# Kernel tuning notes

Measured on AMD Instinct MI355X. Metric: run time of the kernel, lower is better.

## Reference

```python
import jax, jax.numpy as jnp
import numpy as np

DIM = 1024
NUM_HEADS = 16
HEAD_DIM = DIM // NUM_HEADS
SCALE = HEAD_DIM ** -0.5


def setup_inputs() -> dict:
    key = jax.random.key(0)
    ks = jax.random.split(key, 6)
    B, N, C = 2, 2048, DIM
    std = 1.0 / np.sqrt(C)
    x = jax.random.normal(ks[0], (B, N, C), dtype=jnp.float32)
    wq = jax.random.normal(ks[1], (C, C), dtype=jnp.float32) * std
    wk = jax.random.normal(ks[2], (C, C), dtype=jnp.float32) * std
    wv = jax.random.normal(ks[3], (C, C), dtype=jnp.float32) * std
    w_proj = jax.random.normal(ks[4], (C, C), dtype=jnp.float32) * std
    b_proj = jax.random.normal(ks[5], (C,), dtype=jnp.float32) * 0.01
    return {"x": x, "wq": wq, "wk": wk, "wv": wv, "w_proj": w_proj, "b_proj": b_proj}


def reference(x, wq, wk, wv, w_proj, b_proj):
    B, N, C = x.shape
    H, D = NUM_HEADS, HEAD_DIM
    Nq = N // 2
    # q from first half of tokens; k, v from all tokens
    q = (x[:, :Nq] @ wq.T).reshape(B, Nq, H, D).transpose(0, 2, 1, 3)  # [B,H,Nq,D]
    k = (x @ wk.T).reshape(B, N, H, D).transpose(0, 2, 1, 3)           # [B,H,N,D]
    v = (x @ wv.T).reshape(B, N, H, D).transpose(0, 2, 1, 3)           # [B,H,N,D]
    attn = jnp.einsum('bhqd,bhkd->bhqk', q, k) * SCALE
    attn = jax.nn.softmax(attn, axis=-1)
    out = jnp.einsum('bhqk,bhkd->bhqd', attn, v)                       # [B,H,Nq,D]
    out = out.transpose(0, 2, 1, 3).reshape(B, Nq, C)
    return out @ w_proj.T + b_proj
```

## Files before the change

### kernel.cpp

```cpp
#include <hip/hip_runtime.h>

typedef _Float16 f16;
typedef _Float16 f16x8 __attribute__((ext_vector_type(8)));
typedef _Float16 f16x4 __attribute__((ext_vector_type(4)));
typedef float f32x4 __attribute__((ext_vector_type(4)));

#define MFMA_F16(a, b, c) __builtin_amdgcn_mfma_f32_16x16x32_f16(a, b, c, 0, 0, 0)

__device__ __forceinline__ void gld16(const void* g, void* l) {
  __builtin_amdgcn_global_load_lds(
      (const __attribute__((address_space(1))) unsigned int*)(unsigned long long)g,
      (__attribute__((address_space(3))) unsigned int*)(unsigned long long)l, 16, 0, 0);
}

__global__ __launch_bounds__(256) void cvt_x_kernel(const float* __restrict__ in,
                                                    f16* __restrict__ out, int n8) {
  int i = blockIdx.x * 256 + threadIdx.x;
  if (i >= n8) return;
  const float4* p = (const float4*)(in + (size_t)i * 8);
  float4 a = p[0], b = p[1];
  f16x8 o = {(f16)a.x, (f16)a.y, (f16)a.z, (f16)a.w,
             (f16)b.x, (f16)b.y, (f16)b.z, (f16)b.w};
  *(f16x8*)(out + (size_t)i * 8) = o;
}

__global__ __launch_bounds__(256) void cvt_w4_kernel(const float* __restrict__ w0,
                                                     const float* __restrict__ w1,
                                                     const float* __restrict__ w2,
                                                     const float* __restrict__ w3,
                                                     f16* __restrict__ out) {
  int i = blockIdx.x * 256 + threadIdx.x;
  int t = i >> 17, r = i & 131071;
  const float* w = (t == 0) ? w0 : (t == 1) ? w1 : (t == 2) ? w2 : w3;
  const float4* p = (const float4*)(w + (size_t)r * 8);
  float4 a = p[0], b = p[1];
  f16x8 o = {(f16)a.x, (f16)a.y, (f16)a.z, (f16)a.w,
             (f16)b.x, (f16)b.y, (f16)b.z, (f16)b.w};
  *(f16x8*)(out + (size_t)t * 1048576 + (size_t)r * 8) = o;
}

__global__ __launch_bounds__(256) void qkv_gemm_kernel(
    const f16* __restrict__ A, const f16* __restrict__ Wq,
    const f16* __restrict__ Wk, const f16* __restrict__ Wv,
    f16* __restrict__ Qo, f16* __restrict__ Ko, f16* __restrict__ VT) {
  __shared__ __align__(16) f16 As[2][64 * 64];
  __shared__ __align__(16) f16 Bs[2][128 * 64];
  const int bid = blockIdx.x + blockIdx.y * 8;
  const int swz = (bid & 7) * 160 + (bid >> 3);
  const int bx = swz & 7, y = swz >> 3;
  const f16* Bw;
  f16* Co = nullptr;
  int mt, isv = 0;
  if (y < 32) { Bw = Wq; Co = Qo; mt = (y & 15) | ((y >> 4) << 5); }
  else if (y < 96) { Bw = Wk; Co = Ko; mt = y - 32; }
  else { Bw = Wv; isv = 1; mt = y - 96; }
  const int m0 = mt * 64, n0 = bx * 128;
  const int tid = threadIdx.x, lane = tid & 63, w = tid >> 6;
  const int wr = w >> 1, wc = w & 1, g = lane >> 4, c = lane & 15;
  const int r_st = tid >> 3, t_st = tid & 7;

  auto stage = [&](int k0, int buf) {
#pragma unroll
    for (int i = 0; i < 2; ++i) {
      int row = r_st + i * 32;
      int sl = (t_st ^ (row & 7)) * 8;
      gld16(&A[(size_t)(m0 + row) * 1024 + k0 + sl], &As[buf][(row * 8 + t_st) * 8]);
    }
#pragma unroll
    for (int i = 0; i < 4; ++i) {
      int row = r_st + i * 32;
      int sl = (t_st ^ (row & 7)) * 8;
      gld16(&Bw[(size_t)(n0 + row) * 1024 + k0 + sl], &Bs[buf][(row * 8 + t_st) * 8]);
    }
  };

  f32x4 acc[2][4] = {};

  stage(0, 0);
  __syncthreads();

  for (int t = 0; t < 16; ++t) {
    const int cur = t & 1;
    if (t < 15) stage((t + 1) * 64, cur ^ 1);
#pragma unroll
    for (int kb = 0; kb < 2; ++kb) {
      f16x8 af[2], bf[4];
      const int sw = ((kb * 4 + g) ^ (c & 7)) * 8;
#pragma unroll
      for (int m2 = 0; m2 < 2; ++m2)
        af[m2] = *(const f16x8*)&As[cur][(wr * 32 + m2 * 16 + c) * 64 + sw];
#pragma unroll
      for (int nt = 0; nt < 4; ++nt)
        bf[nt] = *(const f16x8*)&Bs[cur][(wc * 64 + nt * 16 + c) * 64 + sw];
#pragma unroll
      for (int m2 = 0; m2 < 2; ++m2)
#pragma unroll
        for (int nt = 0; nt < 4; ++nt)
          acc[m2][nt] = MFMA_F16(af[m2], bf[nt], acc[m2][nt]);
    }
    __syncthreads();
  }

  if (isv) {
    const int b = m0 >> 11;
    const int n_base = (m0 & 2047) + wr * 32 + g * 4;
#pragma unroll
    for (int m2 = 0; m2 < 2; ++m2)
#pragma unroll
      for (int nt = 0; nt < 4; ++nt) {
        int col = n0 + wc * 64 + nt * 16 + c;
        int h = col >> 6, d = col & 63;
        f16x4 pv = {(f16)acc[m2][nt][0], (f16)acc[m2][nt][1],
                    (f16)acc[m2][nt][2], (f16)acc[m2][nt][3]};
        *(f16x4*)&VT[((size_t)((b * 16 + h) * 64 + d)) * 2048 + n_base + m2 * 16] = pv;
      }
  } else {
#pragma unroll
    for (int m2 = 0; m2 < 2; ++m2)
#pragma unroll
      for (int nt = 0; nt < 4; ++nt) {
        int col = n0 + wc * 64 + nt * 16 + c;
#pragma unroll
        for (int r = 0; r < 4; ++r)
          Co[(size_t)(m0 + wr * 32 + m2 * 16 + g * 4 + r) * 1024 + col] =
              (f16)acc[m2][nt][r];
      }
  }
}

__global__ __launch_bounds__(256) void proj_gemm_kernel(
    const f16* __restrict__ A, const f16* __restrict__ Bw,
    float* __restrict__ C) {
  __shared__ __align__(16) f16 As[2][64 * 64];
  __shared__ __align__(16) f16 Bs[2][64 * 64];
  const int bid = blockIdx.x;
  const int swz = (bid & 7) * 128 + (bid >> 3);
  const int n0 = (swz & 15) * 64, m0 = ((swz >> 4) & 31) * 64;
  const int kbase = (swz >> 9) * 512;
  const int tid = threadIdx.x, lane = tid & 63, w = tid >> 6;
  const int wr = w >> 1, wc = w & 1, g = lane >> 4, c = lane & 15;
  const int r_st = tid >> 3, t_st = tid & 7;

  auto stage = [&](int k0, int buf) {
#pragma unroll
    for (int i = 0; i < 2; ++i) {
      int row = r_st + i * 32;
      int sl = (t_st ^ (row & 7)) * 8;
      gld16(&A[(size_t)(m0 + row) * 1024 + k0 + sl], &As[buf][(row * 8 + t_st) * 8]);
      gld16(&Bw[(size_t)(n0 + row) * 1024 + k0 + sl], &Bs[buf][(row * 8 + t_st) * 8]);
    }
  };

  f32x4 acc[2][2] = {};

  stage(kbase, 0);
  __syncthreads();

  for (int t = 0; t < 8; ++t) {
    const int cur = t & 1;
    if (t < 7) stage(kbase + (t + 1) * 64, cur ^ 1);
#pragma unroll
    for (int kb = 0; kb < 2; ++kb) {
      f16x8 af[2], bf[2];
      const int sw = ((kb * 4 + g) ^ (c & 7)) * 8;
#pragma unroll
      for (int m2 = 0; m2 < 2; ++m2)
        af[m2] = *(const f16x8*)&As[cur][(wr * 32 + m2 * 16 + c) * 64 + sw];
#pragma unroll
      for (int nt = 0; nt < 2; ++nt)
        bf[nt] = *(const f16x8*)&Bs[cur][(wc * 32 + nt * 16 + c) * 64 + sw];
#pragma unroll
      for (int m2 = 0; m2 < 2; ++m2)
#pragma unroll
        for (int nt = 0; nt < 2; ++nt)
          acc[m2][nt] = MFMA_F16(af[m2], bf[nt], acc[m2][nt]);
    }
    __syncthreads();
  }

#pragma unroll
  for (int m2 = 0; m2 < 2; ++m2)
#pragma unroll
    for (int nt = 0; nt < 2; ++nt) {
      int col = n0 + wc * 32 + nt * 16 + c;
#pragma unroll
      for (int r = 0; r < 4; ++r)
        unsafeAtomicAdd(&C[(size_t)(m0 + wr * 32 + m2 * 16 + g * 4 + r) * 1024 + col],
                        acc[m2][nt][r]);
    }
}

__global__ __launch_bounds__(256, 3) void attn_kernel(const f16* __restrict__ Q,
                                                      const f16* __restrict__ Kg,
                                                      const f16* __restrict__ VT,
                                                      f16* __restrict__ Opart,
                                                      float* __restrict__ ML) {
  __shared__ __align__(16) f16 Ks[2][64 * 64];
  __shared__ __align__(16) f16 Vs[64 * 64];
  __shared__ __align__(16) f16 Ps[4][32 * 64];
  const int flat = blockIdx.x;
  const int swz = (flat & 7) * 128 + (flat >> 3);
  const int qt = swz & 7, h = (swz >> 3) & 15;
  const int ch = (swz >> 7) & 3, b = swz >> 9;
  const int tid = threadIdx.x, lane = tid & 63, w = tid >> 6;
  const int g = lane >> 4, c = lane & 15;
  const int r_st = tid >> 3, t_st = tid & 7;

  const f16* Kbase = Kg + (size_t)(b * 2048 + ch * 512) * 1024 + h * 64;
  const f16* Vbase = VT + ((size_t)((b * 16 + h) * 64)) * 2048 + ch * 512;

  f16x8 qf[2][2];
#pragma unroll
  for (int qs = 0; qs < 2; ++qs) {
    const f16* qp =
        Q + (size_t)(b * 2048 + qt * 128 + w * 32 + qs * 16 + c) * 1024 + h * 64;
    qf[qs][0] = *(const f16x8*)(qp + g * 8);
    qf[qs][1] = *(const f16x8*)(qp + 32 + g * 8);
#pragma unroll
    for (int j = 0; j < 8; ++j) {
      qf[qs][0][j] = (f16)((float)qf[qs][0][j] * 0.1803368801f);
      qf[qs][1][j] = (f16)((float)qf[qs][1][j] * 0.1803368801f);
    }
  }

  auto stageK = [&](int t, int buf) {
#pragma unroll
    for (int i = 0; i < 2; ++i) {
      int row = r_st + i * 32;
      int sl = (t_st ^ (row & 7)) * 8;
      gld16(&Kbase[(size_t)(t * 64 + row) * 1024 + sl],
            &Ks[buf][(row * 8 + t_st) * 8]);
    }
  };
  auto stageV = [&](int t) {
#pragma unroll
    for (int i = 0; i < 2; ++i) {
      int row = r_st + i * 32;
      int sl = (t_st ^ (row & 7)) * 8;
      gld16(&Vbase[(size_t)row * 2048 + t * 64 + sl], &Vs[(row * 8 + t_st) * 8]);
    }
  };

  f32x4 oaccT[4][2] = {};
  float l_part[2] = {0.f, 0.f};

  stageK(0, 0);
  stageV(0);
  asm volatile("s_waitcnt vmcnt(0)" ::: "memory");
  __builtin_amdgcn_s_barrier();
  __builtin_amdgcn_sched_barrier(0);

  for (int t = 0; t < 8; ++t) {
    const int cur = t & 1;
    if (t < 7) stageK(t + 1, cur ^ 1);

#pragma unroll
    for (int qs = 0; qs < 2; ++qs) {
      f32x4 s[4] = {};
      __builtin_amdgcn_s_setprio(1);
#pragma unroll
      for (int kt = 0; kt < 4; ++kt) {
        f16x8 kf0 =
            *(const f16x8*)&Ks[cur][(kt * 16 + c) * 64 + ((g ^ (c & 7)) * 8)];
        f16x8 kf1 =
            *(const f16x8*)&Ks[cur][(kt * 16 + c) * 64 + (((4 + g) ^ (c & 7)) * 8)];
        s[kt] = MFMA_F16(kf0, qf[qs][0], s[kt]);
        s[kt] = MFMA_F16(kf1, qf[qs][1], s[kt]);
      }
      __builtin_amdgcn_s_setprio(0);
      float rs = 0.f;
#pragma unroll
      for (int kt = 0; kt < 4; ++kt)
#pragma unroll
        for (int r = 0; r < 4; ++r) {
          float p = exp2f(s[kt][r]);
          s[kt][r] = p;
          rs += p;
        }
      l_part[qs] += rs;
#pragma unroll
      for (int kt = 0; kt < 4; ++kt) {
        f16x4 pv = {(f16)s[kt][0], (f16)s[kt][1], (f16)s[kt][2], (f16)s[kt][3]};
        *(f16x4*)&Ps[w][(qs * 16 + c) * 64 +
                        (((kt * 2 + (g >> 1)) ^ (c & 7)) * 8) + (g & 1) * 4] = pv;
      }
    }

    if (t < 7) {
      asm volatile("s_waitcnt vmcnt(2)" ::: "memory");
    } else {
      asm volatile("s_waitcnt vmcnt(0)" ::: "memory");
    }
    __builtin_amdgcn_s_barrier();
    __builtin_amdgcn_sched_barrier(0);

    __builtin_amdgcn_s_setprio(1);
#pragma unroll
    for (int kb = 0; kb < 2; ++kb) {
      f16x8 pf0 =
          *(const f16x8*)&Ps[w][c * 64 + (((kb * 4 + g) ^ (c & 7)) * 8)];
      f16x8 pf1 =
          *(const f16x8*)&Ps[w][(16 + c) * 64 + (((kb * 4 + g) ^ (c & 7)) * 8)];
#pragma unroll
      for (int dt = 0; dt < 4; ++dt) {
        f16x8 vf = *(const f16x8*)&Vs[(dt * 16 + c) * 64 +
                                      (((kb * 4 + g) ^ (c & 7)) * 8)];
        oaccT[dt][0] = MFMA_F16(vf, pf0, oaccT[dt][0]);
        oaccT[dt][1] = MFMA_F16(vf, pf1, oaccT[dt][1]);
      }
    }
    __builtin_amdgcn_s_setprio(0);

    asm volatile("s_waitcnt vmcnt(0)" ::: "memory");
    __builtin_amdgcn_s_barrier();
    __builtin_amdgcn_sched_barrier(0);
    if (t < 7) stageV(t + 1);
  }

  float lf[2];
#pragma unroll
  for (int qs = 0; qs < 2; ++qs) {
    float l = l_part[qs];
    l += __shfl_xor(l, 16);
    l += __shfl_xor(l, 32);
    lf[qs] = l;
  }
#pragma unroll
  for (int qs = 0; qs < 2; ++qs) {
    float li = 1.f / lf[qs];
#pragma unroll
    for (int dt = 0; dt < 4; ++dt) {
      f16x4 ov = {(f16)(oaccT[dt][qs][0] * li), (f16)(oaccT[dt][qs][1] * li),
                  (f16)(oaccT[dt][qs][2] * li), (f16)(oaccT[dt][qs][3] * li)};
      *(f16x4*)&Opart[(size_t)ch * 2097152 +
                      (size_t)(b * 1024 + qt * 128 + w * 32 + qs * 16 + c) * 1024 +
                      h * 64 + dt * 16 + g * 4] = ov;
    }
  }
  if (lane < 16) {
#pragma unroll
    for (int qs = 0; qs < 2; ++qs)
      ML[ch * 32768 + (b * 1024 + qt * 128 + w * 32 + qs * 16 + lane) * 16 + h] =
          lf[qs];
  }
}

__global__ __launch_bounds__(256) void combine_kernel(const f16* __restrict__ Opart,
                                                      const float* __restrict__ ML,
                                                      f16* __restrict__ O16,
                                                      float* __restrict__ outp,
                                                      const float* __restrict__ bias) {
  int i = blockIdx.x * 256 + threadIdx.x;
  int row = i >> 7;
  int h = (i & 127) >> 3;
  float l0 = ML[row * 16 + h];
  float l1 = ML[32768 + row * 16 + h];
  float l2 = ML[65536 + row * 16 + h];
  float l3 = ML[98304 + row * 16 + h];
  float inv = 1.f / (l0 + l1 + l2 + l3);
  f16x8 o0 = *(const f16x8*)&Opart[(size_t)i * 8];
  f16x8 o1 = *(const f16x8*)&Opart[2097152 + (size_t)i * 8];
  f16x8 o2 = *(const f16x8*)&Opart[4194304 + (size_t)i * 8];
  f16x8 o3 = *(const f16x8*)&Opart[6291456 + (size_t)i * 8];
  f16x8 r;
#pragma unroll
  for (int j = 0; j < 8; ++j)
    r[j] = (f16)((l0 * (float)o0[j] + l1 * (float)o1[j] + l2 * (float)o2[j] +
                  l3 * (float)o3[j]) * inv);
  *(f16x8*)&O16[(size_t)i * 8] = r;
  int cb = (i & 127) * 8;
#pragma unroll
  for (int j = 0; j < 8; ++j) outp[(size_t)i * 8 + j] = bias[cb + j];
}

extern "C" void kernel_launch(void* const* d_in, const int* in_sizes, int n_in,
                              void* d_out, int out_size, void* d_ws, size_t ws_size,
                              hipStream_t stream) {
  const float* x = (const float*)d_in[0];
  const float* wq = (const float*)d_in[1];
  const float* wk = (const float*)d_in[2];
  const float* wv = (const float*)d_in[3];
  const float* wp = (const float*)d_in[4];
  const float* bp = (const float*)d_in[5];
  float* out = (float*)d_out;

  char* p = (char*)d_ws;
  f16* x16 = (f16*)p;   p += (size_t)4194304 * 2;
  f16* w16 = (f16*)p;   p += (size_t)4 * 1048576 * 2;
  f16* Q16 = (f16*)p;   p += (size_t)4194304 * 2;
  f16* K16 = (f16*)p;   p += (size_t)4194304 * 2;
  f16* VT16 = (f16*)p;  p += (size_t)4194304 * 2;
  f16* Opart = (f16*)p; p += (size_t)8388608 * 2;
  f16* O16 = (f16*)p;   p += (size_t)2097152 * 2;

  f16* wq16 = w16;
  f16* wk16 = w16 + 1048576;
  f16* wv16 = w16 + 2 * 1048576;
  f16* wp16 = w16 + 3 * 1048576;

  cvt_x_kernel<<<4194304 / 8 / 256, 256, 0, stream>>>(x, x16, 4194304 / 8);
  cvt_w4_kernel<<<4 * 131072 / 256, 256, 0, stream>>>(wq, wk, wv, wp, w16);

  qkv_gemm_kernel<<<dim3(8, 160), 256, 0, stream>>>(x16, wq16, wk16, wv16, Q16, K16,
                                                    VT16);

  float* MLp = (float*)x16;
  attn_kernel<<<dim3(1024), 256, 0, stream>>>(Q16, K16, VT16, Opart, MLp);
  combine_kernel<<<1024, 256, 0, stream>>>(Opart, MLp, O16, out, bp);

  proj_gemm_kernel<<<dim3(1024), 256, 0, stream>>>(O16, wp16, out);
}
```

Before: 99.98 us.

## Retile QKV GEMM to 128x128 blocks with BK=32 and hoist K-fragment loads in attention

The QKV projection GEMM moves from 64x128 tiles with BK=64 to 128x128 tiles with BK=32. Each wave now computes a 64x64 sub-tile, which raises arithmetic intensity per LDS fragment load and halves the grid to 640 blocks. The kernel gets a launch_bounds occupancy hint, and the LDS swizzle is adapted to 4 chunks per row. In the attention kernel, the K fragments are loaded from LDS once per tile and reused for both query sub-blocks instead of being reloaded, and the s_setprio hints are removed. The larger accumulator raises register pressure, and the smaller grid and shorter K-steps with more barriers may hurt latency hiding.

Result: slower. 106.9 us (+6.9%).

```diff
diff --git a/kernel.cpp b/kernel.cpp
--- a/kernel.cpp
+++ b/kernel.cpp
@@ -39,73 +39,65 @@
   *(f16x8*)(out + (size_t)t * 1048576 + (size_t)r * 8) = o;
 }
 
-__global__ __launch_bounds__(256) void qkv_gemm_kernel(
+__global__ __launch_bounds__(256, 5) void qkv_gemm_kernel(
     const f16* __restrict__ A, const f16* __restrict__ Wq,
     const f16* __restrict__ Wk, const f16* __restrict__ Wv,
     f16* __restrict__ Qo, f16* __restrict__ Ko, f16* __restrict__ VT) {
-  __shared__ __align__(16) f16 As[2][64 * 64];
-  __shared__ __align__(16) f16 Bs[2][128 * 64];
+  __shared__ __align__(16) f16 As[2][128 * 32];
+  __shared__ __align__(16) f16 Bs[2][128 * 32];
   const int bid = blockIdx.x + blockIdx.y * 8;
-  const int swz = (bid & 7) * 160 + (bid >> 3);
+  const int swz = (bid & 7) * 80 + (bid >> 3);
   const int bx = swz & 7, y = swz >> 3;
   const f16* Bw;
   f16* Co = nullptr;
   int mt, isv = 0;
-  if (y < 32) { Bw = Wq; Co = Qo; mt = (y & 15) | ((y >> 4) << 5); }
-  else if (y < 96) { Bw = Wk; Co = Ko; mt = y - 32; }
-  else { Bw = Wv; isv = 1; mt = y - 96; }
-  const int m0 = mt * 64, n0 = bx * 128;
+  if (y < 16) { Bw = Wq; Co = Qo; mt = (y & 7) | ((y >> 3) << 4); }
+  else if (y < 48) { Bw = Wk; Co = Ko; mt = y - 16; }
+  else { Bw = Wv; isv = 1; mt = y - 48; }
+  const int m0 = mt * 128, n0 = bx * 128;
   const int tid = threadIdx.x, lane = tid & 63, w = tid >> 6;
   const int wr = w >> 1, wc = w & 1, g = lane >> 4, c = lane & 15;
-  const int r_st = tid >> 3, t_st = tid & 7;
+  const int r_st = tid >> 2, t_st = tid & 3;
 
   auto stage = [&](int k0, int buf) {
 #pragma unroll
     for (int i = 0; i < 2; ++i) {
-      int row = r_st + i * 32;
-      int sl = (t_st ^ (row & 7)) * 8;
-      gld16(&A[(size_t)(m0 + row) * 1024 + k0 + sl], &As[buf][(row * 8 + t_st) * 8]);
-    }
-#pragma unroll
-    for (int i = 0; i < 4; ++i) {
-      int row = r_st + i * 32;
-      int sl = (t_st ^ (row & 7)) * 8;
-      gld16(&Bw[(size_t)(n0 + row) * 1024 + k0 + sl], &Bs[buf][(row * 8 + t_st) * 8]);
+      int row = r_st + i * 64;
+      int sl = (t_st ^ (row & 3)) * 8;
+      gld16(&A[(size_t)(m0 + row) * 1024 + k0 + sl], &As[buf][(row * 4 + t_st) * 8]);
+      gld16(&Bw[(size_t)(n0 + row) * 1024 + k0 + sl], &Bs[buf][(row * 4 + t_st) * 8]);
     }
   };
 
-  f32x4 acc[2][4] = {};
+  f32x4 acc[4][4] = {};
 
   stage(0, 0);
   __syncthreads();
 
-  for (int t = 0; t < 16; ++t) {
+  for (int t = 0; t < 32; ++t) {
     const int cur = t & 1;
-    if (t < 15) stage((t + 1) * 64, cur ^ 1);
-#pragma unroll
-    for (int kb = 0; kb < 2; ++kb) {
-      f16x8 af[2], bf[4];
-      const int sw = ((kb * 4 + g) ^ (c & 7)) * 8;
-#pragma unroll
-      for (int m2 = 0; m2 < 2; ++m2)
-        af[m2] = *(const f16x8*)&As[cur][(wr * 32 + m2 * 16 + c) * 64 + sw];
+    if (t < 31) stage((t + 1) * 32, cur ^ 1);
+    f16x8 af[4], bf[4];
+    const int sw = (g ^ (c & 3)) * 8;
+#pragma unroll
+    for (int m2 = 0; m2 < 4; ++m2)
+      af[m2] = *(const f16x8*)&As[cur][(wr * 64 + m2 * 16 + c) * 32 + sw];
+#pragma unroll
+    for (int nt = 0; nt < 4; ++nt)
+      bf[nt] = *(const f16x8*)&Bs[cur][(wc * 64 + nt * 16 + c) * 32 + sw];
+#pragma unroll
+    for (int m2 = 0; m2 < 4; ++m2)
 #pragma unroll
       for (int nt = 0; nt < 4; ++nt)
-        bf[nt] = *(const f16x8*)&Bs[cur][(wc * 64 + nt * 16 + c) * 64 + sw];
-#pragma unroll
-      for (int m2 = 0; m2 < 2; ++m2)
-#pragma unroll
-        for (int nt = 0; nt < 4; ++nt)
-          acc[m2][nt] = MFMA_F16(af[m2], bf[nt], acc[m2][nt]);
-    }
+        acc[m2][nt] = MFMA_F16(af[m2], bf[nt], acc[m2][nt]);
     __syncthreads();
   }
 
   if (isv) {
     const int b = m0 >> 11;
-    const int n_base = (m0 & 2047) + wr * 32 + g * 4;
-#pragma unroll
-    for (int m2 = 0; m2 < 2; ++m2)
+    const int n_base = (m0 & 2047) + wr * 64 + g * 4;
+#pragma unroll
+    for (int m2 = 0; m2 < 4; ++m2)
 #pragma unroll
       for (int nt = 0; nt < 4; ++nt) {
         int col = n0 + wc * 64 + nt * 16 + c;
@@ -116,13 +108,13 @@
       }
   } else {
 #pragma unroll
-    for (int m2 = 0; m2 < 2; ++m2)
+    for (int m2 = 0; m2 < 4; ++m2)
 #pragma unroll
       for (int nt = 0; nt < 4; ++nt) {
         int col = n0 + wc * 64 + nt * 16 + c;
 #pragma unroll
         for (int r = 0; r < 4; ++r)
-          Co[(size_t)(m0 + wr * 32 + m2 * 16 + g * 4 + r) * 1024 + col] =
+          Co[(size_t)(m0 + wr * 64 + m2 * 16 + g * 4 + r) * 1024 + col] =
               (f16)acc[m2][nt][r];
       }
   }
@@ -254,28 +246,29 @@
     const int cur = t & 1;
     if (t < 7) stageK(t + 1, cur ^ 1);
 
+    f16x8 kf[4][2];
+#pragma unroll
+    for (int kt = 0; kt < 4; ++kt) {
+      kf[kt][0] = *(const f16x8*)&Ks[cur][(kt * 16 + c) * 64 + ((g ^ (c & 7)) * 8)];
+      kf[kt][1] =
+          *(const f16x8*)&Ks[cur][(kt * 16 + c) * 64 + (((4 + g) ^ (c & 7)) * 8)];
+    }
+
 #pragma unroll
     for (int qs = 0; qs < 2; ++qs) {
       f32x4 s[4] = {};
-      __builtin_amdgcn_s_setprio(1);
 #pragma unroll
       for (int kt = 0; kt < 4; ++kt) {
-        f16x8 kf0 =
-            *(const f16x8*)&Ks[cur][(kt * 16 + c) * 64 + ((g ^ (c & 7)) * 8)];
-        f16x8 kf1 =
-            *(const f16x8*)&Ks[cur][(kt * 16 + c) * 64 + (((4 + g) ^ (c & 7)) * 8)];
-        s[kt] = MFMA_F16(kf0, qf[qs][0], s[kt]);
-        s[kt] = MFMA_F16(kf1, qf[qs][1], s[kt]);
+        s[kt] = MFMA_F16(kf[kt][0], qf[qs][0], s[kt]);
+        s[kt] = MFMA_F16(kf[kt][1], qf[qs][1], s[kt]);
       }
-      __builtin_amdgcn_s_setprio(0);
       float rs = 0.f;
 #pragma unroll
       for (int kt = 0; kt < 4; ++kt)
 #pragma unroll
         for (int r = 0; r < 4; ++r) {
-          float p = exp2f(s[kt][r]);
-          s[kt][r] = p;
-          rs += p;
+          s[kt][r] = exp2f(s[kt][r]);
+          rs += s[kt][r];
         }
       l_part[qs] += rs;
 #pragma unroll
@@ -294,11 +287,9 @@
     __builtin_amdgcn_s_barrier();
     __builtin_amdgcn_sched_barrier(0);
 
-    __builtin_amdgcn_s_setprio(1);
 #pragma unroll
     for (int kb = 0; kb < 2; ++kb) {
-      f16x8 pf0 =
-          *(const f16x8*)&Ps[w][c * 64 + (((kb * 4 + g) ^ (c & 7)) * 8)];
+      f16x8 pf0 = *(const f16x8*)&Ps[w][c * 64 + (((kb * 4 + g) ^ (c & 7)) * 8)];
       f16x8 pf1 =
           *(const f16x8*)&Ps[w][(16 + c) * 64 + (((kb * 4 + g) ^ (c & 7)) * 8)];
 #pragma unroll
@@ -309,7 +300,6 @@
         oaccT[dt][1] = MFMA_F16(vf, pf1, oaccT[dt][1]);
       }
     }
-    __builtin_amdgcn_s_setprio(0);
 
     asm volatile("s_waitcnt vmcnt(0)" ::: "memory");
     __builtin_amdgcn_s_barrier();
@@ -401,8 +391,8 @@
   cvt_x_kernel<<<4194304 / 8 / 256, 256, 0, stream>>>(x, x16, 4194304 / 8);
   cvt_w4_kernel<<<4 * 131072 / 256, 256, 0, stream>>>(wq, wk, wv, wp, w16);
 
-  qkv_gemm_kernel<<<dim3(8, 160), 256, 0, stream>>>(x16, wq16, wk16, wv16, Q16, K16,
-                                                    VT16);
+  qkv_gemm_kernel<<<dim3(8, 80), 256, 0, stream>>>(x16, wq16, wk16, wv16, Q16, K16,
+                                                   VT16);
 
   float* MLp = (float*)x16;
   attn_kernel<<<dim3(1024), 256, 0, stream>>>(Q16, K16, VT16, Opart, MLp);
```
